# Optimization experiments

Hardware: AMD Instinct MI355X
Metric: run time of the kernel (lower is better)

## Reference

```python
import jax, jax.numpy as jnp
import numpy as np

V, NJ, NB, NP, NK = 6890, 24, 10, 207, 19
PARENTS = [-1,0,0,0,1,2,3,4,5,6,7,8,9,9,9,12,13,14,16,17,18,19,20,21]


def setup_inputs() -> dict:
    key = jax.random.key(0)
    ks = jax.random.split(key, 9)
    N = 2048
    return {
        "beta": jax.random.normal(ks[0], (N, NB), jnp.float32),
        "theta": jax.random.normal(ks[1], (N, NJ, 3), jnp.float32) * 0.2,
        "trans": jax.random.normal(ks[2], (N, 3), jnp.float32),
        "shapedirs": jax.random.normal(ks[3], (V, 3, NB), jnp.float32) * 0.03,
        "v_template": jax.random.normal(ks[4], (V, 3), jnp.float32),
        "J_regressor": jax.random.uniform(ks[5], (NJ, V), jnp.float32) / V,
        "posedirs": jax.random.normal(ks[6], (V, 3, NP), jnp.float32) * 0.01,
        "weights": jax.nn.softmax(jax.random.normal(ks[7], (V, NJ), jnp.float32) * 4.0, axis=-1),
        "joint_regressor": jax.random.uniform(ks[8], (V, NK), jnp.float32) / V,
    }


def rodrigues(r):
    # r: [M,3] axis-angle -> [M,3,3] rotation matrices
    theta = jnp.maximum(jnp.linalg.norm(r, axis=-1, keepdims=True),
                        jnp.finfo(r.dtype).tiny)  # [M,1]
    rh = r / theta
    c = jnp.cos(theta)[:, :, None]  # [M,1,1]
    s = jnp.sin(theta)[:, :, None]
    z = jnp.zeros_like(rh[:, 0])
    K = jnp.stack([z, -rh[:, 2], rh[:, 1],
                   rh[:, 2], z, -rh[:, 0],
                   -rh[:, 1], rh[:, 0], z], axis=1).reshape(-1, 3, 3)
    outer = rh[:, :, None] * rh[:, None, :]
    return c * jnp.eye(3, dtype=r.dtype) + (1.0 - c) * outer + s * K


def reference(beta, theta, trans, shapedirs, v_template, J_regressor, posedirs, weights, joint_regressor):
    N = beta.shape[0]
    dt = beta.dtype
    v_shaped = jnp.einsum('nb,vcb->nvc', beta, shapedirs) + v_template  # [N,V,3]
    J = jnp.einsum('jv,nvc->njc', J_regressor, v_shaped)                # [N,24,3]
    # pose rotations and pose blendshapes
    R = rodrigues(theta.reshape(-1, 3)).reshape(N, NJ, 3, 3)
    lrotmin = (R[:, 1:] - jnp.eye(3, dtype=dt)).reshape(N, NP)
    v_posed = v_shaped + jnp.einsum('np,vcp->nvc', lrotmin, posedirs)
    # kinematic chain: 24 small 4x4 transforms with parent dependencies
    bottom = jnp.broadcast_to(jnp.array([0., 0., 0., 1.], dtype=dt), (N, 1, 4))
    def make_A(Ri, t):  # [N,3,3],[N,3] -> [N,4,4]
        return jnp.concatenate([jnp.concatenate([Ri, t[:, :, None]], axis=2), bottom], axis=1)
    G = [make_A(R[:, 0], J[:, 0])]
    for i in range(1, NJ):
        p = PARENTS[i]
        G.append(G[p] @ make_A(R[:, i], J[:, i] - J[:, p]))
    G = jnp.stack(G, axis=1)  # [N,24,4,4]
    # subtract rest-pose joint contribution
    Jh = jnp.concatenate([J, jnp.zeros((N, NJ, 1), dt)], axis=2)[..., None]  # [N,24,4,1]
    corr = G @ Jh
    G_rel = G - jnp.concatenate([jnp.zeros((N, NJ, 4, 3), dt), corr], axis=3)
    # linear blend skinning
    T = jnp.einsum('njab,vj->nvab', G_rel, weights)  # [N,V,4,4]
    vh = jnp.concatenate([v_posed, jnp.ones((N, V, 1), dt)], axis=2)  # [N,V,4]
    v = jnp.einsum('nvab,nvb->nva', T, vh)[..., :3]
    verts = v + trans[:, None, :]
    joints = jnp.einsum('nvc,vk->nkc', verts, joint_regressor)  # [N,19,3]
    return verts, joints
```

## Files before the change

kernel.cpp:

```cpp
#include <hip/hip_runtime.h>

#define V      6890
#define NJ     24
#define NB     10
#define NP     207
#define NK     19
#define NBATCH 2048
#define KP     224
#define KC     217
#define VC     (V*3)
#define VCP    20736
#define BN     64
#define BV     64
#define VST4   260
#define VSEG   1723
#define JSP    18
#define JCH    9

using bh8   = __attribute__((ext_vector_type(8))) short;
using u16x4 = __attribute__((ext_vector_type(4))) unsigned short;
using f32x4 = __attribute__((ext_vector_type(4))) float;

__constant__ int PAR[NJ] = {-1,0,0,0,1,2,3,4,5,6,7,8,9,9,9,12,13,14,16,17,18,19,20,21};

__device__ __forceinline__ unsigned short f2bf(float f) {
    unsigned int u = __float_as_uint(f);
    u += 0x7FFFu + ((u >> 16) & 1u);
    return (unsigned short)(u >> 16);
}
__device__ __forceinline__ float bf2f(unsigned short h) {
    return __uint_as_float((unsigned int)h << 16);
}

__global__ __launch_bounds__(256) void k_prep(const float* __restrict__ Jreg,
                                              const float* __restrict__ vtmpl,
                                              const float* __restrict__ sdirs,
                                              const float* __restrict__ pdirs,
                                              const float* __restrict__ jreg,
                                              float* __restrict__ JB,
                                              unsigned short* __restrict__ Bmat,
                                              unsigned short* __restrict__ JbigT) {
    int blk = blockIdx.x, tid = threadIdx.x;
    if (blk < 792) {
        int vs = blk & 3, og = blk >> 2;
        int o = og*4 + (tid >> 6);
        int lane = tid & 63;
        int j = o/33, t = o%33, c = t/11, m = t%11;
        int lo = vs*VSEG + lane, hi = min(V, vs*VSEG + VSEG);
        const float* jr = Jreg + j*V;
        float s = 0.f;
        if (m == 0) { for (int v = lo; v < hi; v += 64) s += jr[v] * vtmpl[v*3 + c]; }
        else        { for (int v = lo; v < hi; v += 64) s += jr[v] * sdirs[(v*3 + c)*NB + (m-1)]; }
        #pragma unroll
        for (int d = 1; d < 64; d <<= 1) s += __shfl_xor(s, d);
        if (lane == 0) atomicAdd(&JB[(j*3 + c)*11 + m], s);
    } else if (blk < 792 + 18144) {
        int gid = (blk - 792)*256 + tid;
        int vc = gid / KP, k = gid - vc*KP;
        float val;
        if (vc >= VC)     val = 0.f;
        else if (k < NB)  val = sdirs[vc*NB + k];
        else if (k < KC)  val = pdirs[vc*NP + (k - NB)];
        else if (k == KC) val = vtmpl[vc];
        else              val = 0.f;
        Bmat[((size_t)(k >> 5)*VCP + vc)*32 + (k & 31)] = f2bf(val);
    } else {
        int gid = (blk - 792 - 18144)*256 + tid;
        int kc = gid / VCP, vc = gid - kc*VCP;
        float val = 0.f;
        if (kc < NK*3 && vc < VC && (kc % 3) == (vc % 3))
            val = jreg[(vc/3)*NK + (kc/3)];
        JbigT[((size_t)(vc >> 5)*64 + kc)*32 + (vc & 31)] = f2bf(val);
    }
}

__global__ __launch_bounds__(64) void k_pern(const float* __restrict__ beta,
                                             const float* __restrict__ theta,
                                             const float* __restrict__ trans,
                                             const float* __restrict__ JB,
                                             unsigned short* __restrict__ Arow,
                                             unsigned short* __restrict__ Gt) {
    int n = blockIdx.x, tid = threadIdx.x;
    __shared__ float Rsm[NJ][9];
    __shared__ float Jsm[NJ][3];
    __shared__ float Gsm[NJ][12];

    if (tid < NJ) {
        const float* th = theta + (n*NJ + tid)*3;
        float x = th[0], y = th[1], z = th[2];
        float nrm = sqrtf(x*x + y*y + z*z);
        float t = fmaxf(nrm, 1.1754944e-38f);
        float inv = 1.0f / t;
        float rx = x*inv, ry = y*inv, rz = z*inv;
        float c = cosf(t), s = sinf(t), oc = 1.0f - c;
        Rsm[tid][0] = c + oc*rx*rx;      Rsm[tid][1] = oc*rx*ry - s*rz;  Rsm[tid][2] = oc*rx*rz + s*ry;
        Rsm[tid][3] = oc*ry*rx + s*rz;   Rsm[tid][4] = c + oc*ry*ry;     Rsm[tid][5] = oc*ry*rz - s*rx;
        Rsm[tid][6] = oc*rz*rx - s*ry;   Rsm[tid][7] = oc*rz*ry + s*rx;  Rsm[tid][8] = c + oc*rz*rz;
    } else if (tid < 2*NJ) {
        int j = tid - NJ;
        #pragma unroll
        for (int c = 0; c < 3; ++c) {
            float s = JB[(j*3+c)*11 + 0];
            #pragma unroll
            for (int b = 0; b < NB; ++b) s += JB[(j*3+c)*11 + 1 + b] * beta[n*NB + b];
            Jsm[j][c] = s;
        }
    }
    __syncthreads();

    if (tid < 12) {
        int a = tid >> 2, b = tid & 3;
        Gsm[0][a*4+b] = (b < 3) ? Rsm[0][a*3+b] : Jsm[0][a];
    }
    __syncthreads();
    for (int i = 1; i < NJ; ++i) {
        if (tid < 12) {
            int a = tid >> 2, b = tid & 3;
            int p = PAR[i];
            float acc = (b == 3) ? Gsm[p][a*4+3] : 0.0f;
            #pragma unroll
            for (int k = 0; k < 3; ++k) {
                float aval = (b < 3) ? Rsm[i][k*3+b] : (Jsm[i][k] - Jsm[p][k]);
                acc += Gsm[p][a*4+k] * aval;
            }
            Gsm[i][a*4+b] = acc;
        }
        __syncthreads();
    }
    if (tid < NJ) {
        int j = tid;
        #pragma unroll
        for (int a = 0; a < 3; ++a) {
            float t3 = Gsm[j][a*4+3]
                     - (Gsm[j][a*4+0]*Jsm[j][0] + Gsm[j][a*4+1]*Jsm[j][1] + Gsm[j][a*4+2]*Jsm[j][2])
                     + trans[n*3 + a];
            Gsm[j][a*4+3] = t3;
        }
    }
    __syncthreads();
    unsigned short* gt = Gt + n*512;
    for (int idx = tid; idx < 512; idx += 64) {
        int e = idx >> 5, j = idx & 31;
        float val = (e < 12 && j < NJ) ? Gsm[j][e] : 0.0f;
        gt[idx] = f2bf(val);
    }
    for (int k = tid; k < KP; k += 64) {
        float val;
        if (k < NB) val = beta[n*NB + k];
        else if (k < KC) {
            int p = k - NB; int jj = p/9 + 1; int rr = p%9;
            val = Rsm[jj][rr] - ((rr==0 || rr==4 || rr==8) ? 1.0f : 0.0f);
        } else if (k == KC) val = 1.0f;
        else val = 0.0f;
        Arow[((size_t)(k >> 5)*NBATCH + n)*32 + (k & 31)] = f2bf(val);
    }
}

__global__ __launch_bounds__(512) void k_main(const unsigned short* __restrict__ Arow,
                                              const unsigned short* __restrict__ Bmat,
                                              const unsigned short* __restrict__ Gt,
                                              const float* __restrict__ weights,
                                              float* __restrict__ verts) {
    __shared__ __attribute__((aligned(16))) unsigned short vhsm[BN*VST4];

    int tid = threadIdx.x;
    int wv = tid >> 6, lane = tid & 63;
    int l15 = lane & 15, jg = lane >> 4;
    int wn = wv >> 2, wc = wv & 3;
    int nb = blockIdx.x, vb = blockIdx.y;
    int n0 = nb * BN, v0 = vb * BV, vc0 = v0 * 3;

    int c4[3];
    #pragma unroll
    for (int ct = 0; ct < 3; ++ct) {
        int vcw = wc*48 + ct*16 + l15;
        c4[ct] = (vcw/3)*4 + vcw%3;
    }
    int tri = (((lane % 3)*16) + lane/3) * 4;

    const unsigned short* abase = Arow + ((size_t)(n0 + wn*32) + l15)*32 + jg*8;
    const unsigned short* bbase = Bmat + ((size_t)(vc0 + wc*48) + l15)*32 + jg*8;
    f32x4 acc[2][3] = {};
    #pragma unroll
    for (int ks = 0; ks < 7; ++ks) {
        bh8 a[2], b[3];
        #pragma unroll
        for (int mt = 0; mt < 2; ++mt)
            a[mt] = *(const bh8*)(abase + (size_t)ks*NBATCH*32 + mt*16*32);
        #pragma unroll
        for (int ct = 0; ct < 3; ++ct)
            b[ct] = *(const bh8*)(bbase + (size_t)ks*VCP*32 + ct*16*32);
        #pragma unroll
        for (int mt = 0; mt < 2; ++mt)
            #pragma unroll
            for (int ct = 0; ct < 3; ++ct)
                acc[mt][ct] = __builtin_amdgcn_mfma_f32_16x16x32_bf16(a[mt], b[ct], acc[mt][ct], 0, 0, 0);
    }

    #pragma unroll
    for (int mt = 0; mt < 2; ++mt)
        #pragma unroll
        for (int ct = 0; ct < 3; ++ct)
            #pragma unroll
            for (int r = 0; r < 4; ++r)
                vhsm[(wn*32 + mt*16 + jg*4 + r)*VST4 + c4[ct]] = f2bf(acc[mt][ct][r]);
    __syncthreads();

    bh8 wfrag[4];
    #pragma unroll
    for (int mt = 0; mt < 4; ++mt) {
        int vr = v0 + mt*16 + l15;
        bh8 f = {0,0,0,0,0,0,0,0};
        if (jg < 3 && vr < V) {
            const float4* wp = (const float4*)(weights + (size_t)vr*NJ + jg*8);
            float4 w0 = wp[0], w1 = wp[1];
            f[0]=(short)f2bf(w0.x); f[1]=(short)f2bf(w0.y); f[2]=(short)f2bf(w0.z); f[3]=(short)f2bf(w0.w);
            f[4]=(short)f2bf(w1.x); f[5]=(short)f2bf(w1.y); f[6]=(short)f2bf(w1.z); f[7]=(short)f2bf(w1.w);
        }
        wfrag[mt] = f;
    }

    const unsigned short* gbase = Gt + ((size_t)(n0 + wv*8))*512 + l15*32 + jg*8;
    #pragma unroll
    for (int nl = 0; nl < 8; ++nl) {
        bh8 gfr = *(const bh8*)(gbase + nl*512);
        int n_loc = wv*8 + nl;
        #pragma unroll
        for (int mt = 0; mt < 4; ++mt) {
            f32x4 z = {0.f, 0.f, 0.f, 0.f};
            f32x4 t = __builtin_amdgcn_mfma_f32_16x16x32_bf16(gfr, wfrag[mt], z, 0, 0, 0);
            u16x4 vh4 = *(const u16x4*)&vhsm[n_loc*VST4 + (mt*16 + l15)*4];
            float p = t[0]*bf2f(vh4[0]) + t[1]*bf2f(vh4[1]) + t[2]*bf2f(vh4[2]) + t[3];
            float pp = __int_as_float(__builtin_amdgcn_ds_bpermute(tri, __float_as_int(p)));
            int col = vc0 + mt*48 + lane;
            if (lane < 48 && col < VC)
                verts[(size_t)(n0 + n_loc)*VC + col] = pp;
        }
    }
}

__global__ __launch_bounds__(256) void k_joints(const float* __restrict__ verts,
                                                const unsigned short* __restrict__ JbigT,
                                                float* __restrict__ joints) {
    __shared__ __attribute__((aligned(16))) unsigned short vt[32*128];

    int tid = threadIdx.x;
    int lane = tid & 63, wv = tid >> 6;
    int l15 = lane & 15, jg = lane >> 4;
    int nt = blockIdx.x, ks = blockIdx.y;
    int n0 = nt * 32;
    int step0 = ks * (JCH*4);

    int row[4], c4[4];
    #pragma unroll
    for (int i = 0; i < 4; ++i) {
        int idx = i*256 + tid;
        row[i] = idx >> 5; c4[i] = idx & 31;
    }

    float2 rg[8];
    auto issue = [&](int ch) {
        int k0f = (step0 + ch*4) * 32;
        #pragma unroll
        for (int i = 0; i < 4; ++i) {
            const float* p = verts + (size_t)(n0 + row[i])*VC + k0f + c4[i]*4;
            rg[2*i+0] = *(const float2*)(p);
            rg[2*i+1] = *(const float2*)(p+2);
        }
    };

    issue(0);
    f32x4 acc[2] = {};
    #pragma unroll 1
    for (int ch = 0; ch < JCH; ++ch) {
        __syncthreads();
        #pragma unroll
        for (int i = 0; i < 4; ++i) {
            u16x4 w;
            w[0] = f2bf(rg[2*i].x); w[1] = f2bf(rg[2*i].y);
            w[2] = f2bf(rg[2*i+1].x); w[3] = f2bf(rg[2*i+1].y);
            int sidx = (row[i]*128 + c4[i]*4) ^ ((row[i] & 7) << 3);
            *(u16x4*)&vt[sidx] = w;
        }
        __syncthreads();
        if (ch + 1 < JCH) issue(ch + 1);
        #pragma unroll
        for (int kk = 0; kk < 4; ++kk) {
            int r0 = l15, r1 = 16 + l15;
            bh8 a0 = *(const bh8*)&vt[(r0*128 + kk*32 + jg*8) ^ ((r0 & 7) << 3)];
            bh8 a1 = *(const bh8*)&vt[(r1*128 + kk*32 + jg*8) ^ ((r1 & 7) << 3)];
            bh8 b  = *(const bh8*)(JbigT + ((size_t)(step0 + ch*4 + kk)*64 + wv*16 + l15)*32 + jg*8);
            acc[0] = __builtin_amdgcn_mfma_f32_16x16x32_bf16(a0, b, acc[0], 0, 0, 0);
            acc[1] = __builtin_amdgcn_mfma_f32_16x16x32_bf16(a1, b, acc[1], 0, 0, 0);
        }
    }
    int kc = wv*16 + l15;
    if (kc < NK*3) {
        #pragma unroll
        for (int mt = 0; mt < 2; ++mt)
            #pragma unroll
            for (int r = 0; r < 4; ++r)
                atomicAdd(&joints[(size_t)(n0 + mt*16 + jg*4 + r)*(NK*3) + kc], acc[mt][r]);
    }
}

extern "C" void kernel_launch(void* const* d_in, const int* in_sizes, int n_in,
                              void* d_out, int out_size, void* d_ws, size_t ws_size,
                              hipStream_t stream) {
    const float* beta  = (const float*)d_in[0];
    const float* theta = (const float*)d_in[1];
    const float* trans = (const float*)d_in[2];
    const float* sdirs = (const float*)d_in[3];
    const float* vtmpl = (const float*)d_in[4];
    const float* jregJ = (const float*)d_in[5];
    const float* pdirs = (const float*)d_in[6];
    const float* wgts  = (const float*)d_in[7];
    const float* jregK = (const float*)d_in[8];

    float* verts  = (float*)d_out;
    float* joints = verts + (size_t)NBATCH * VC;

    char* ws = (char*)d_ws;
    float*          JB    = (float*)ws;
    unsigned short* Arow  = (unsigned short*)(ws + 4096);
    unsigned short* Gt    = (unsigned short*)(ws + 4096 + 917504);
    unsigned short* Bmat  = (unsigned short*)(ws + 4096 + 917504 + 2097152);
    unsigned short* JbigT = (unsigned short*)(ws + 4096 + 917504 + 2097152 + 9289728);

    hipMemsetAsync(JB, 0, 4096, stream);
    hipMemsetAsync(joints, 0, (size_t)NBATCH*NK*3*sizeof(float), stream);

    k_prep <<<792 + 18144 + 5184, 256, 0, stream>>>(jregJ, vtmpl, sdirs, pdirs, jregK, JB, Bmat, JbigT);
    k_pern <<<NBATCH, 64, 0, stream>>>(beta, theta, trans, JB, Arow, Gt);
    dim3 g4(NBATCH/BN, (V + BV - 1)/BV);
    k_main <<<g4, 512, 0, stream>>>(Arow, Bmat, Gt, wgts, verts);
    dim3 g5(NBATCH/32, JSP);
    k_joints<<<g5, 256, 0, stream>>>(verts, JbigT, joints);
}
```

Baseline: 166.3 us.

## Vectorize prep packing, stage B via LDS in main GEMM, replace joint atomics with reduction

The prep kernel now has each thread pack eight bf16 values and write them with one 16-byte store, where before each thread wrote one element. The main kernel loads B tiles through global_load_lds into per-wave LDS buffers and prefetches A and B for the next k-step while the current MFMAs run. The joints kernel writes partial sums to a workspace and a new reduction kernel adds them, which replaces the float atomics and the output memset. The costs are an extra launch, more LDS use per block, and explicit waitcnt barriers that may serialize the load-use sequence.

After: 159.8 us. 1.04x faster.

```diff
diff --git a/kernel.cpp b/kernel.cpp
--- a/kernel.cpp
+++ b/kernel.cpp
@@ -16,9 +16,11 @@
 #define VSEG   1723
 #define JSP    18
 #define JCH    9
+#define BWSZ   1536
 
 using bh8   = __attribute__((ext_vector_type(8))) short;
 using u16x4 = __attribute__((ext_vector_type(4))) unsigned short;
+using u16x8 = __attribute__((ext_vector_type(8))) unsigned short;
 using f32x4 = __attribute__((ext_vector_type(4))) float;
 
 __constant__ int PAR[NJ] = {-1,0,0,0,1,2,3,4,5,6,7,8,9,9,9,12,13,14,16,17,18,19,20,21};
@@ -54,23 +56,47 @@
         #pragma unroll
         for (int d = 1; d < 64; d <<= 1) s += __shfl_xor(s, d);
         if (lane == 0) atomicAdd(&JB[(j*3 + c)*11 + m], s);
-    } else if (blk < 792 + 18144) {
+    } else if (blk < 792 + 2268) {
         int gid = (blk - 792)*256 + tid;
-        int vc = gid / KP, k = gid - vc*KP;
-        float val;
-        if (vc >= VC)     val = 0.f;
-        else if (k < NB)  val = sdirs[vc*NB + k];
-        else if (k < KC)  val = pdirs[vc*NP + (k - NB)];
-        else if (k == KC) val = vtmpl[vc];
-        else              val = 0.f;
-        Bmat[((size_t)(k >> 5)*VCP + vc)*32 + (k & 31)] = f2bf(val);
+        int vc = gid / 28, q = gid - vc*28;
+        int k0 = q*8;
+        unsigned short out[8];
+        if (vc >= VC) {
+            #pragma unroll
+            for (int j = 0; j < 8; ++j) out[j] = 0;
+        } else if (q >= 2 && q <= 26) {
+            const float* p = pdirs + (size_t)vc*NP + (k0 - NB);
+            #pragma unroll
+            for (int j = 0; j < 8; ++j) out[j] = f2bf(p[j]);
+        } else {
+            #pragma unroll
+            for (int j = 0; j < 8; ++j) {
+                int k = k0 + j;
+                float val;
+                if (k < NB)       val = sdirs[vc*NB + k];
+                else if (k < KC)  val = pdirs[(size_t)vc*NP + (k - NB)];
+                else if (k == KC) val = vtmpl[vc];
+                else              val = 0.f;
+                out[j] = f2bf(val);
+            }
+        }
+        *(u16x8*)&Bmat[((size_t)(k0 >> 5)*VCP + vc)*32 + (k0 & 31)] = *(u16x8*)out;
     } else {
-        int gid = (blk - 792 - 18144)*256 + tid;
-        int kc = gid / VCP, vc = gid - kc*VCP;
-        float val = 0.f;
-        if (kc < NK*3 && vc < VC && (kc % 3) == (vc % 3))
-            val = jreg[(vc/3)*NK + (kc/3)];
-        JbigT[((size_t)(vc >> 5)*64 + kc)*32 + (vc & 31)] = f2bf(val);
+        int gid = (blk - 792 - 2268)*256 + tid;
+        int kc = gid / (VCP/8), u = gid - kc*(VCP/8);
+        int vc0 = u*8;
+        unsigned short out[8];
+        #pragma unroll
+        for (int j = 0; j < 8; ++j) out[j] = 0;
+        if (kc < NK*3) {
+            #pragma unroll
+            for (int j = 0; j < 8; ++j) {
+                int vc = vc0 + j;
+                if (vc < VC && (vc % 3) == (kc % 3))
+                    out[j] = f2bf(jreg[(vc/3)*NK + (kc/3)]);
+            }
+        }
+        *(u16x8*)&JbigT[((size_t)(vc0 >> 5)*64 + kc)*32 + (vc0 & 31)] = *(u16x8*)out;
     }
 }
 
@@ -161,6 +187,7 @@
                                               const unsigned short* __restrict__ Gt,
                                               const float* __restrict__ weights,
                                               float* __restrict__ verts) {
+    __shared__ __attribute__((aligned(16))) unsigned short Bw[8*BWSZ];
     __shared__ __attribute__((aligned(16))) unsigned short vhsm[BN*VST4];
 
     int tid = threadIdx.x;
@@ -178,23 +205,45 @@
     }
     int tri = (((lane % 3)*16) + lane/3) * 4;
 
+    unsigned short* bwbase = &Bw[wv*BWSZ];
+    const unsigned short* bsrc0 = Bmat + ((size_t)(vc0 + wc*48))*32;
+    auto stageB = [&](int ks) {
+        const unsigned short* s = bsrc0 + (size_t)ks*VCP*32;
+        #pragma unroll
+        for (int i = 0; i < 3; ++i) {
+            __builtin_amdgcn_global_load_lds(
+                (const __attribute__((address_space(1))) void*)(s + i*512 + (size_t)lane*8),
+                (__attribute__((address_space(3))) void*)(bwbase + i*512),
+                16, 0, 0);
+        }
+    };
+
     const unsigned short* abase = Arow + ((size_t)(n0 + wn*32) + l15)*32 + jg*8;
-    const unsigned short* bbase = Bmat + ((size_t)(vc0 + wc*48) + l15)*32 + jg*8;
+    stageB(0);
+    bh8 a0 = *(const bh8*)(abase);
+    bh8 a1 = *(const bh8*)(abase + 16*32);
     f32x4 acc[2][3] = {};
     #pragma unroll
     for (int ks = 0; ks < 7; ++ks) {
-        bh8 a[2], b[3];
-        #pragma unroll
-        for (int mt = 0; mt < 2; ++mt)
-            a[mt] = *(const bh8*)(abase + (size_t)ks*NBATCH*32 + mt*16*32);
-        #pragma unroll
-        for (int ct = 0; ct < 3; ++ct)
-            b[ct] = *(const bh8*)(bbase + (size_t)ks*VCP*32 + ct*16*32);
-        #pragma unroll
-        for (int mt = 0; mt < 2; ++mt)
-            #pragma unroll
-            for (int ct = 0; ct < 3; ++ct)
-                acc[mt][ct] = __builtin_amdgcn_mfma_f32_16x16x32_bf16(a[mt], b[ct], acc[mt][ct], 0, 0, 0);
+        asm volatile("s_waitcnt vmcnt(0)" ::: "memory");
+        __builtin_amdgcn_sched_barrier(0);
+        bh8 b0 = *(const bh8*)(bwbase + ( 0 + l15)*32 + jg*8);
+        bh8 b1 = *(const bh8*)(bwbase + (16 + l15)*32 + jg*8);
+        bh8 b2 = *(const bh8*)(bwbase + (32 + l15)*32 + jg*8);
+        asm volatile("s_waitcnt lgkmcnt(0)" ::: "memory");
+        __builtin_amdgcn_sched_barrier(0);
+        bh8 a0c = a0, a1c = a1;
+        if (ks < 6) {
+            stageB(ks + 1);
+            a0 = *(const bh8*)(abase + (size_t)(ks+1)*NBATCH*32);
+            a1 = *(const bh8*)(abase + (size_t)(ks+1)*NBATCH*32 + 16*32);
+        }
+        acc[0][0] = __builtin_amdgcn_mfma_f32_16x16x32_bf16(a0c, b0, acc[0][0], 0, 0, 0);
+        acc[0][1] = __builtin_amdgcn_mfma_f32_16x16x32_bf16(a0c, b1, acc[0][1], 0, 0, 0);
+        acc[0][2] = __builtin_amdgcn_mfma_f32_16x16x32_bf16(a0c, b2, acc[0][2], 0, 0, 0);
+        acc[1][0] = __builtin_amdgcn_mfma_f32_16x16x32_bf16(a1c, b0, acc[1][0], 0, 0, 0);
+        acc[1][1] = __builtin_amdgcn_mfma_f32_16x16x32_bf16(a1c, b1, acc[1][1], 0, 0, 0);
+        acc[1][2] = __builtin_amdgcn_mfma_f32_16x16x32_bf16(a1c, b2, acc[1][2], 0, 0, 0);
     }
 
     #pragma unroll
@@ -241,7 +290,7 @@
 
 __global__ __launch_bounds__(256) void k_joints(const float* __restrict__ verts,
                                                 const unsigned short* __restrict__ JbigT,
-                                                float* __restrict__ joints) {
+                                                float* __restrict__ jpart) {
     __shared__ __attribute__((aligned(16))) unsigned short vt[32*128];
 
     int tid = threadIdx.x;
@@ -294,14 +343,24 @@
             acc[1] = __builtin_amdgcn_mfma_f32_16x16x32_bf16(a1, b, acc[1], 0, 0, 0);
         }
     }
-    int kc = wv*16 + l15;
-    if (kc < NK*3) {
-        #pragma unroll
-        for (int mt = 0; mt < 2; ++mt)
-            #pragma unroll
-            for (int r = 0; r < 4; ++r)
-                atomicAdd(&joints[(size_t)(n0 + mt*16 + jg*4 + r)*(NK*3) + kc], acc[mt][r]);
-    }
+    float* jp = jpart + ((size_t)ks*NBATCH + n0)*64 + wv*16 + l15;
+    #pragma unroll
+    for (int mt = 0; mt < 2; ++mt)
+        #pragma unroll
+        for (int r = 0; r < 4; ++r)
+            jp[(size_t)(mt*16 + jg*4 + r)*64] = acc[mt][r];
+}
+
+__global__ __launch_bounds__(256) void k_jred(const float* __restrict__ jpart,
+                                              float* __restrict__ joints) {
+    int idx = blockIdx.x*256 + threadIdx.x;
+    if (idx >= NBATCH*NK*3) return;
+    int n = idx / (NK*3), i = idx - n*(NK*3);
+    float s = 0.f;
+    #pragma unroll
+    for (int ks = 0; ks < JSP; ++ks)
+        s += jpart[((size_t)ks*NBATCH + n)*64 + i];
+    joints[idx] = s;
 }
 
 extern "C" void kernel_launch(void* const* d_in, const int* in_sizes, int n_in,
@@ -326,14 +385,15 @@
     unsigned short* Gt    = (unsigned short*)(ws + 4096 + 917504);
     unsigned short* Bmat  = (unsigned short*)(ws + 4096 + 917504 + 2097152);
     unsigned short* JbigT = (unsigned short*)(ws + 4096 + 917504 + 2097152 + 9289728);
+    float*          jpart = (float*)(ws + 4096 + 917504 + 2097152 + 9289728 + 2654208);
 
     hipMemsetAsync(JB, 0, 4096, stream);
-    hipMemsetAsync(joints, 0, (size_t)NBATCH*NK*3*sizeof(float), stream);
-
-    k_prep <<<792 + 18144 + 5184, 256, 0, stream>>>(jregJ, vtmpl, sdirs, pdirs, jregK, JB, Bmat, JbigT);
+
+    k_prep <<<792 + 2268 + 648, 256, 0, stream>>>(jregJ, vtmpl, sdirs, pdirs, jregK, JB, Bmat, JbigT);
     k_pern <<<NBATCH, 64, 0, stream>>>(beta, theta, trans, JB, Arow, Gt);
     dim3 g4(NBATCH/BN, (V + BV - 1)/BV);
     k_main <<<g4, 512, 0, stream>>>(Arow, Bmat, Gt, wgts, verts);
     dim3 g5(NBATCH/32, JSP);
-    k_joints<<<g5, 256, 0, stream>>>(verts, JbigT, joints);
-}
+    k_joints<<<g5, 256, 0, stream>>>(verts, JbigT, jpart);
+    k_jred <<<(NBATCH*NK*3 + 255)/256, 256, 0, stream>>>(jpart, joints);
+}
```
